# Kernel optimization log

Measured on AMD Instinct MI355X. Metric: run time of the kernel, lower is better.

Reference implementation:

```python
import jax, jax.numpy as jnp
from jax import lax
import numpy as np

L2 = 1.0   # regularization_strength for soft_rank
W1 = 1.0   # weight on (1 - spearman)
W2 = 1.0   # weight on BCE-with-logits


def _isotonic_nondecreasing(y):
    """argmin_{v1<=...<=vn} 0.5||v-y||^2 via the min-max (pool means) formula.
    v_i = max_{j<=i} min_{k>=i} mean(y[j..k]). Same solution (and generic
    gradient) as sequential PAV, but fully vectorized / O(n^2)."""
    n = y.shape[0]
    c = jnp.concatenate([jnp.zeros((1,), y.dtype), jnp.cumsum(y)])  # prefix sums
    j = jnp.arange(n)[:, None]
    k = jnp.arange(n)[None, :]
    length = (k - j + 1).astype(y.dtype)
    M = (c[k + 1] - c[j]) / length                    # mean(y[j..k]) for j<=k
    BIG = jnp.asarray(np.finfo(np.float32).max / 4, y.dtype)
    M = jnp.where(j <= k, M, BIG)                     # mask invalid j>k
    S = lax.cummin(M, axis=1, reverse=True)           # S[j,i] = min_{k>=i} M[j,k]
    V = lax.cummax(S, axis=0)                         # V[i,i] = max_{j<=i} S[j,i]
    return jnp.diagonal(V)


def _isotonic_nonincreasing(y):
    # argmin_{v1>=...>=vn} 0.5||v-y||^2  (what fast_soft_sort's isotonic_l2 solves)
    return -_isotonic_nondecreasing(-y)


def _soft_rank_1d(x, reg):
    """fast_soft_sort soft_rank (L2 regularization, ASCENDING) for a 1D vector:
    projection of x/reg onto the permutahedron of w=[n,...,1]."""
    n = x.shape[0]
    theta = x / reg
    w = jnp.arange(n, 0, -1, dtype=x.dtype)           # [n, n-1, ..., 1]
    perm = jnp.argsort(-theta)                        # descending sort
    s = theta[perm]
    dual = _isotonic_nonincreasing(s - w)
    primal = s - dual
    inv = jnp.argsort(perm)
    return primal[inv]


def setup_inputs() -> dict:
    key = jax.random.key(0)
    k1, k2 = jax.random.split(key)
    y_hat = jax.random.normal(k1, (1, 4096), dtype=jnp.float32)   # logits
    y = jax.random.uniform(k2, (1, 4096), dtype=jnp.float32)      # targets in [0,1]
    return {"y_hat": y_hat, "y": y}


def reference(y_hat, y):
    sr = jax.vmap(lambda v: _soft_rank_1d(v, L2))     # rank each row
    p = sr(y_hat)
    t = sr(y)
    p = p - p.mean()
    p = p / jnp.linalg.norm(p)
    t = t - t.mean()
    t = t / jnp.linalg.norm(t)
    spearman = jnp.sum(p * t)
    # BCEWithLogitsLoss (mean reduction): mean(log(1+exp(x)) - x*y), stable form
    bce = jnp.mean(jnp.logaddexp(0.0, y_hat) - y_hat * y)
    return W1 * (1.0 - spearman) + W2 * bce
```

## Files before the change

### kernel.cpp

```cpp
#include <hip/hip_runtime.h>
#include <math.h>

#define N 4096

__global__ __launch_bounds__(256) void rank_kernel(
        const float* __restrict__ yh, const float* __restrict__ yv,
        float* __restrict__ sA, float* __restrict__ sB,
        int* __restrict__ posA, int* __restrict__ posB) {
    int g = blockIdx.x * 256 + threadIdx.x;
    int elem = g >> 3;
    int k = g & 7;
    int row = elem >> 12;
    int i = elem & (N - 1);
    const float* X = row ? yv : yh;
    float x = X[i];
    const float4* X4 = (const float4*)X;
    int cnt = 0;
    int m0 = k * 128;
#pragma unroll 4
    for (int m = m0; m < m0 + 128; ++m) {
        float4 f = X4[m];
        int j = 4 * m;
        cnt += (int)(f.x > x) | ((int)(f.x == x) & (int)((j + 0) < i));
        cnt += (int)(f.y > x) | ((int)(f.y == x) & (int)((j + 1) < i));
        cnt += (int)(f.z > x) | ((int)(f.z == x) & (int)((j + 2) < i));
        cnt += (int)(f.w > x) | ((int)(f.w == x) & (int)((j + 3) < i));
    }
    cnt += __shfl_xor(cnt, 1, 8);
    cnt += __shfl_xor(cnt, 2, 8);
    cnt += __shfl_xor(cnt, 4, 8);
    if (k == 0) {
        if (row) { posB[i] = cnt; sB[cnt] = x; }
        else     { posA[i] = cnt; sA[cnt] = x; }
    }
}

__global__ __launch_bounds__(1024) void finalize_kernel(
        const float* __restrict__ yh, const float* __restrict__ yv,
        const float* __restrict__ sA, const float* __restrict__ sB,
        const int* __restrict__ posA, const int* __restrict__ posB,
        float* __restrict__ out) {
    __shared__ double wtot[2][8];
    __shared__ double CNsh[2];
    __shared__ unsigned short survX[2][512];
    __shared__ double survY[2][512];
    __shared__ unsigned short gX[2][516];
    __shared__ double gY[2][516];
    __shared__ double gSlope[2][516];
    __shared__ int survCnt[2];
    __shared__ int Hsh[2];
    __shared__ double wred[16][6];

    const int tid  = threadIdx.x;
    const int lane = tid & 63;
    const int wave = tid >> 6;
    const int r    = tid >> 9;
    const int ht   = tid & 511;
    const int hw   = wave & 7;
    const int q0   = ht * 8;

    int4 pa4 = ((const int4*)posA)[tid];
    int4 pb4 = ((const int4*)posB)[tid];
    float4 xh = ((const float4*)yh)[tid];
    float4 yt = ((const float4*)yv)[tid];

    const float* S = r ? sB : sA;
    float4 sa4 = ((const float4*)S)[2 * ht];
    float4 sb4 = ((const float4*)S)[2 * ht + 1];
    float sv[8] = {sa4.x, sa4.y, sa4.z, sa4.w, sb4.x, sb4.y, sb4.z, sb4.w};

    double m[8];
    double acc = 0.0;
#pragma unroll
    for (int j = 0; j < 8; ++j) {
        acc += (double)sv[j] - (double)(N - (q0 + j));
        m[j] = acc;
    }
    double tot = m[7], incl = tot;
#pragma unroll
    for (int d = 1; d < 64; d <<= 1) {
        double t = __shfl_up(incl, d, 64);
        if (lane >= d) incl += t;
    }
    if (lane == 63) wtot[r][hw] = incl;
    if (tid < 2) survCnt[tid] = 0;
    __syncthreads();

    if (tid < 16) {
        int rr = tid >> 3, idx = tid & 7;
        double v = wtot[rr][idx], inc = v;
#pragma unroll
        for (int d = 1; d < 8; d <<= 1) {
            double t = __shfl_up(inc, d, 8);
            if (idx >= d) inc += t;
        }
        wtot[rr][idx] = inc - v;
        if (idx == 7) CNsh[rr] = inc;
    }
    __syncthreads();

    double base = wtot[r][hw] + (incl - tot);
    double CN = CNsh[r];
    double eps = 1e-9 * fabs(CN) + 1e-6;
    const double invN = 1.0 / (double)N;

#pragma unroll
    for (int j = 0; j < 8; ++j) {
        int p = q0 + 1 + j;
        if (p < N) {
            double cp = base + m[j];
            if (cp > CN * ((double)p * invN) - eps) {
                int slot = atomicAdd(&survCnt[r], 1);
                if (slot < 512) { survX[r][slot] = (unsigned short)p; survY[r][slot] = cp; }
            }
        }
    }
    __syncthreads();

    if (ht == 0) {
        int k = survCnt[r]; if (k > 512) k = 512;
        for (int a = 1; a < k; ++a) {
            unsigned short vx = survX[r][a]; double vy = survY[r][a];
            int b = a - 1;
            while (b >= 0 && survX[r][b] > vx) {
                survX[r][b + 1] = survX[r][b]; survY[r][b + 1] = survY[r][b]; --b;
            }
            survX[r][b + 1] = vx; survY[r][b + 1] = vy;
        }
        int cnt = 0;
        int xa = 0, xb = 0; double ya = 0.0, yb = 0.0;
        for (int q = 0; q <= k + 1; ++q) {
            int x; double cy;
            if (q == 0)      { x = 0; cy = 0.0; }
            else if (q <= k) { x = (int)survX[r][q - 1]; cy = survY[r][q - 1]; }
            else             { x = N; cy = CN; }
            while (cnt >= 2) {
                double cr = (double)(xb - xa) * (cy - ya) - (yb - ya) * (double)(x - xa);
                if (cr >= 0.0) {
                    cnt--; xb = xa; yb = ya;
                    if (cnt >= 2) { xa = (int)gX[r][cnt - 2]; ya = gY[r][cnt - 2]; }
                } else break;
            }
            gX[r][cnt] = (unsigned short)x; gY[r][cnt] = cy;
            xa = xb; ya = yb; xb = x; yb = cy;
            cnt++;
        }
        Hsh[r] = cnt;
        for (int q = 0; q + 1 < cnt; ++q)
            gSlope[r][q] = (gY[r][q + 1] - gY[r][q]) /
                           (double)((int)gX[r][q + 1] - (int)gX[r][q]);
    }
    __syncthreads();

    double Sa = 0, Sb = 0, Saa = 0, Sbb = 0, Sab = 0, Bce = 0;
    {
        int HA = Hsh[0], HB = Hsh[1];
        int pa[4] = {pa4.x, pa4.y, pa4.z, pa4.w};
        int pb[4] = {pb4.x, pb4.y, pb4.z, pb4.w};
        float xx[4] = {xh.x, xh.y, xh.z, xh.w};
        float yy[4] = {yt.x, yt.y, yt.z, yt.w};
#pragma unroll
        for (int j = 0; j < 4; ++j) {
            int p = pa[j];
            int a = 0, b2 = HA - 1;
            while (b2 - a > 1) {
                int mm = (a + b2) >> 1;
                if ((int)gX[0][mm] <= p) a = mm; else b2 = mm;
            }
            double dualA = gSlope[0][a];
            p = pb[j];
            a = 0; b2 = HB - 1;
            while (b2 - a > 1) {
                int mm = (a + b2) >> 1;
                if ((int)gX[1][mm] <= p) a = mm; else b2 = mm;
            }
            double dualB = gSlope[1][a];

            double av = (double)xx[j] - dualA - 2048.0;
            double bv = (double)yy[j] - dualB - 2048.0;
            Sa += av; Sb += bv; Saa += av * av; Sbb += bv * bv; Sab += av * bv;
            float x = xx[j];
            float e = __expf(-fabsf(x));
            float bt = fmaxf(x, 0.0f) + __logf(1.0f + e) - x * yy[j];
            Bce += (double)bt;
        }
    }
#pragma unroll
    for (int d = 32; d; d >>= 1) {
        Sa  += __shfl_xor(Sa, d, 64);  Sb  += __shfl_xor(Sb, d, 64);
        Saa += __shfl_xor(Saa, d, 64); Sbb += __shfl_xor(Sbb, d, 64);
        Sab += __shfl_xor(Sab, d, 64); Bce += __shfl_xor(Bce, d, 64);
    }
    if (lane == 0) {
        wred[wave][0] = Sa;  wred[wave][1] = Sb;  wred[wave][2] = Saa;
        wred[wave][3] = Sbb; wred[wave][4] = Sab; wred[wave][5] = Bce;
    }
    __syncthreads();
    if (tid == 0) {
        double sa = 0, sb = 0, saa = 0, sbb = 0, sab = 0, bce = 0;
        for (int w = 0; w < 16; ++w) {
            sa += wred[w][0]; sb += wred[w][1]; saa += wred[w][2];
            sbb += wred[w][3]; sab += wred[w][4]; bce += wred[w][5];
        }
        double n = (double)N;
        double cov = sab - sa * sb / n;
        double va = saa - sa * sa / n;
        double vb = sbb - sb * sb / n;
        double spearman = cov / sqrt(va * vb);
        out[0] = (float)(1.0 - spearman + bce / n);
    }
}

extern "C" void kernel_launch(void* const* d_in, const int* in_sizes, int n_in,
                              void* d_out, int out_size, void* d_ws, size_t ws_size,
                              hipStream_t stream) {
    const float* yh = (const float*)d_in[0];
    const float* yv = (const float*)d_in[1];
    float* out = (float*)d_out;

    float* sA  = (float*)d_ws;
    float* sB  = sA + N;
    int* posA  = (int*)(sB + N);
    int* posB  = posA + N;

    hipLaunchKernelGGL(rank_kernel, dim3(256), dim3(256), 0, stream,
                       yh, yv, sA, sB, posA, posB);
    hipLaunchKernelGGL(finalize_kernel, dim3(1), dim3(1024), 0, stream,
                       yh, yv, sA, sB, posA, posB, out);
}
```

Before: 78.50 us.

## Fuse rank and finalize kernels into one cooperative launch with grid sync

Merges the counting-rank kernel and the single-block finalize kernel into one cooperative kernel, separated by a grid-wide sync. Block 0 then runs the finalize step with 256 threads instead of 1024, so each thread handles 32 sorted values and 16 elements. The goal is to drop the second launch and the gap between kernels. In exchange, the grid sync has its own cost, and the finalize step now has less parallelism and longer serial loops per thread, including many sequential atomics.

```diff
diff --git a/kernel.cpp b/kernel.cpp
--- a/kernel.cpp
+++ b/kernel.cpp
@@ -1,47 +1,52 @@
 #include <hip/hip_runtime.h>
+#include <hip/hip_cooperative_groups.h>
 #include <math.h>
 
 #define N 4096
 
-__global__ __launch_bounds__(256) void rank_kernel(
+namespace cg = cooperative_groups;
+
+__global__ __launch_bounds__(256) void fused_kernel(
         const float* __restrict__ yh, const float* __restrict__ yv,
         float* __restrict__ sA, float* __restrict__ sB,
-        int* __restrict__ posA, int* __restrict__ posB) {
-    int g = blockIdx.x * 256 + threadIdx.x;
-    int elem = g >> 3;
-    int k = g & 7;
-    int row = elem >> 12;
-    int i = elem & (N - 1);
-    const float* X = row ? yv : yh;
-    float x = X[i];
-    const float4* X4 = (const float4*)X;
-    int cnt = 0;
-    int m0 = k * 128;
+        int* __restrict__ posA, int* __restrict__ posB,
+        float* __restrict__ out) {
+    {
+        int g = blockIdx.x * 256 + threadIdx.x;
+        int elem = g >> 3;
+        int k = g & 7;
+        int row = elem >> 12;
+        int i = elem & (N - 1);
+        const float* X = row ? yv : yh;
+        float x = X[i];
+        const float4* X4 = (const float4*)X;
+        int cnt = 0;
+        int m0 = k * 128;
 #pragma unroll 4
-    for (int m = m0; m < m0 + 128; ++m) {
-        float4 f = X4[m];
-        int j = 4 * m;
-        cnt += (int)(f.x > x) | ((int)(f.x == x) & (int)((j + 0) < i));
-        cnt += (int)(f.y > x) | ((int)(f.y == x) & (int)((j + 1) < i));
-        cnt += (int)(f.z > x) | ((int)(f.z == x) & (int)((j + 2) < i));
-        cnt += (int)(f.w > x) | ((int)(f.w == x) & (int)((j + 3) < i));
-    }
-    cnt += __shfl_xor(cnt, 1, 8);
-    cnt += __shfl_xor(cnt, 2, 8);
-    cnt += __shfl_xor(cnt, 4, 8);
-    if (k == 0) {
-        if (row) { posB[i] = cnt; sB[cnt] = x; }
-        else     { posA[i] = cnt; sA[cnt] = x; }
-    }
-}
-
-__global__ __launch_bounds__(1024) void finalize_kernel(
-        const float* __restrict__ yh, const float* __restrict__ yv,
-        const float* __restrict__ sA, const float* __restrict__ sB,
-        const int* __restrict__ posA, const int* __restrict__ posB,
-        float* __restrict__ out) {
-    __shared__ double wtot[2][8];
-    __shared__ double CNsh[2];
+        for (int m = m0; m < m0 + 128; ++m) {
+            float4 f = X4[m];
+            int j = 4 * m;
+            cnt += (int)(f.x > x) | ((int)(f.x == x) & (int)((j + 0) < i));
+            cnt += (int)(f.y > x) | ((int)(f.y == x) & (int)((j + 1) < i));
+            cnt += (int)(f.z > x) | ((int)(f.z == x) & (int)((j + 2) < i));
+            cnt += (int)(f.w > x) | ((int)(f.w == x) & (int)((j + 3) < i));
+        }
+        cnt += __shfl_xor(cnt, 1, 8);
+        cnt += __shfl_xor(cnt, 2, 8);
+        cnt += __shfl_xor(cnt, 4, 8);
+        if (k == 0) {
+            if (row) { posB[i] = cnt; sB[cnt] = x; }
+            else     { posA[i] = cnt; sA[cnt] = x; }
+        }
+    }
+
+    __threadfence();
+    cg::this_grid().sync();
+
+    if (blockIdx.x != 0) return;
+    __threadfence();
+
+    __shared__ double wT[4];
     __shared__ unsigned short survX[2][512];
     __shared__ double survY[2][512];
     __shared__ unsigned short gX[2][516];
@@ -49,77 +54,78 @@
     __shared__ double gSlope[2][516];
     __shared__ int survCnt[2];
     __shared__ int Hsh[2];
-    __shared__ double wred[16][6];
+    __shared__ double wred[4][6];
 
     const int tid  = threadIdx.x;
     const int lane = tid & 63;
     const int wave = tid >> 6;
-    const int r    = tid >> 9;
-    const int ht   = tid & 511;
-    const int hw   = wave & 7;
-    const int q0   = ht * 8;
-
-    int4 pa4 = ((const int4*)posA)[tid];
-    int4 pb4 = ((const int4*)posB)[tid];
-    float4 xh = ((const float4*)yh)[tid];
-    float4 yt = ((const float4*)yv)[tid];
+    const int r    = tid >> 7;
+    const int t    = tid & 127;
+    const int q0   = t * 32;
+
+    int4 pa4[4], pb4[4]; float4 xh4[4], yt4[4];
+#pragma unroll
+    for (int u = 0; u < 4; ++u) {
+        pa4[u] = ((const int4*)posA)[4 * tid + u];
+        pb4[u] = ((const int4*)posB)[4 * tid + u];
+        xh4[u] = ((const float4*)yh)[4 * tid + u];
+        yt4[u] = ((const float4*)yv)[4 * tid + u];
+    }
 
     const float* S = r ? sB : sA;
-    float4 sa4 = ((const float4*)S)[2 * ht];
-    float4 sb4 = ((const float4*)S)[2 * ht + 1];
-    float sv[8] = {sa4.x, sa4.y, sa4.z, sa4.w, sb4.x, sb4.y, sb4.z, sb4.w};
-
-    double m[8];
+    float4 sv4[8];
+#pragma unroll
+    for (int u = 0; u < 8; ++u) sv4[u] = ((const float4*)S)[8 * t + u];
+
     double acc = 0.0;
 #pragma unroll
-    for (int j = 0; j < 8; ++j) {
-        acc += (double)sv[j] - (double)(N - (q0 + j));
-        m[j] = acc;
-    }
-    double tot = m[7], incl = tot;
+    for (int u = 0; u < 8; ++u) {
+        int q = q0 + 4 * u;
+        acc += (double)sv4[u].x - (double)(N - (q + 0));
+        acc += (double)sv4[u].y - (double)(N - (q + 1));
+        acc += (double)sv4[u].z - (double)(N - (q + 2));
+        acc += (double)sv4[u].w - (double)(N - (q + 3));
+    }
+    double tot = acc, incl = acc;
 #pragma unroll
     for (int d = 1; d < 64; d <<= 1) {
-        double t = __shfl_up(incl, d, 64);
-        if (lane >= d) incl += t;
-    }
-    if (lane == 63) wtot[r][hw] = incl;
+        double tt = __shfl_up(incl, d, 64);
+        if (lane >= d) incl += tt;
+    }
+    if (lane == 63) wT[wave] = incl;
     if (tid < 2) survCnt[tid] = 0;
     __syncthreads();
 
-    if (tid < 16) {
-        int rr = tid >> 3, idx = tid & 7;
-        double v = wtot[rr][idx], inc = v;
-#pragma unroll
-        for (int d = 1; d < 8; d <<= 1) {
-            double t = __shfl_up(inc, d, 8);
-            if (idx >= d) inc += t;
-        }
-        wtot[rr][idx] = inc - v;
-        if (idx == 7) CNsh[rr] = inc;
-    }
-    __syncthreads();
-
-    double base = wtot[r][hw] + (incl - tot);
-    double CN = CNsh[r];
+    double wprev = (wave & 1) ? wT[wave - 1] : 0.0;
+    double CN = wT[2 * r] + wT[2 * r + 1];
+    double base = wprev + (incl - tot);
     double eps = 1e-9 * fabs(CN) + 1e-6;
     const double invN = 1.0 / (double)N;
 
-#pragma unroll
-    for (int j = 0; j < 8; ++j) {
-        int p = q0 + 1 + j;
-        if (p < N) {
-            double cp = base + m[j];
-            if (cp > CN * ((double)p * invN) - eps) {
-                int slot = atomicAdd(&survCnt[r], 1);
-                if (slot < 512) { survX[r][slot] = (unsigned short)p; survY[r][slot] = cp; }
-            }
-        }
-    }
-    __syncthreads();
-
-    if (ht == 0) {
-        int k = survCnt[r]; if (k > 512) k = 512;
-        for (int a = 1; a < k; ++a) {
+    {
+        double cp = base;
+#pragma unroll
+        for (int u = 0; u < 8; ++u) {
+            float fv[4] = {sv4[u].x, sv4[u].y, sv4[u].z, sv4[u].w};
+#pragma unroll
+            for (int c = 0; c < 4; ++c) {
+                int q = q0 + 4 * u + c;
+                cp += (double)fv[c] - (double)(N - q);
+                int p = q + 1;
+                if (p < N && cp > CN * ((double)p * invN) - eps) {
+                    int slot = atomicAdd(&survCnt[r], 1);
+                    if (slot < 512) {
+                        survX[r][slot] = (unsigned short)p; survY[r][slot] = cp;
+                    }
+                }
+            }
+        }
+    }
+    __syncthreads();
+
+    if (t == 0) {
+        int kk = survCnt[r]; if (kk > 512) kk = 512;
+        for (int a = 1; a < kk; ++a) {
             unsigned short vx = survX[r][a]; double vy = survY[r][a];
             int b = a - 1;
             while (b >= 0 && survX[r][b] > vx) {
@@ -127,26 +133,26 @@
             }
             survX[r][b + 1] = vx; survY[r][b + 1] = vy;
         }
-        int cnt = 0;
+        int cnt2 = 0;
         int xa = 0, xb = 0; double ya = 0.0, yb = 0.0;
-        for (int q = 0; q <= k + 1; ++q) {
+        for (int q = 0; q <= kk + 1; ++q) {
             int x; double cy;
-            if (q == 0)      { x = 0; cy = 0.0; }
-            else if (q <= k) { x = (int)survX[r][q - 1]; cy = survY[r][q - 1]; }
-            else             { x = N; cy = CN; }
-            while (cnt >= 2) {
+            if (q == 0)       { x = 0; cy = 0.0; }
+            else if (q <= kk) { x = (int)survX[r][q - 1]; cy = survY[r][q - 1]; }
+            else              { x = N; cy = CN; }
+            while (cnt2 >= 2) {
                 double cr = (double)(xb - xa) * (cy - ya) - (yb - ya) * (double)(x - xa);
                 if (cr >= 0.0) {
-                    cnt--; xb = xa; yb = ya;
-                    if (cnt >= 2) { xa = (int)gX[r][cnt - 2]; ya = gY[r][cnt - 2]; }
+                    cnt2--; xb = xa; yb = ya;
+                    if (cnt2 >= 2) { xa = (int)gX[r][cnt2 - 2]; ya = gY[r][cnt2 - 2]; }
                 } else break;
             }
-            gX[r][cnt] = (unsigned short)x; gY[r][cnt] = cy;
+            gX[r][cnt2] = (unsigned short)x; gY[r][cnt2] = cy;
             xa = xb; ya = yb; xb = x; yb = cy;
-            cnt++;
-        }
-        Hsh[r] = cnt;
-        for (int q = 0; q + 1 < cnt; ++q)
+            cnt2++;
+        }
+        Hsh[r] = cnt2;
+        for (int q = 0; q + 1 < cnt2; ++q)
             gSlope[r][q] = (gY[r][q + 1] - gY[r][q]) /
                            (double)((int)gX[r][q + 1] - (int)gX[r][q]);
     }
@@ -155,34 +161,37 @@
     double Sa = 0, Sb = 0, Saa = 0, Sbb = 0, Sab = 0, Bce = 0;
     {
         int HA = Hsh[0], HB = Hsh[1];
-        int pa[4] = {pa4.x, pa4.y, pa4.z, pa4.w};
-        int pb[4] = {pb4.x, pb4.y, pb4.z, pb4.w};
-        float xx[4] = {xh.x, xh.y, xh.z, xh.w};
-        float yy[4] = {yt.x, yt.y, yt.z, yt.w};
-#pragma unroll
-        for (int j = 0; j < 4; ++j) {
-            int p = pa[j];
-            int a = 0, b2 = HA - 1;
-            while (b2 - a > 1) {
-                int mm = (a + b2) >> 1;
-                if ((int)gX[0][mm] <= p) a = mm; else b2 = mm;
-            }
-            double dualA = gSlope[0][a];
-            p = pb[j];
-            a = 0; b2 = HB - 1;
-            while (b2 - a > 1) {
-                int mm = (a + b2) >> 1;
-                if ((int)gX[1][mm] <= p) a = mm; else b2 = mm;
-            }
-            double dualB = gSlope[1][a];
-
-            double av = (double)xx[j] - dualA - 2048.0;
-            double bv = (double)yy[j] - dualB - 2048.0;
-            Sa += av; Sb += bv; Saa += av * av; Sbb += bv * bv; Sab += av * bv;
-            float x = xx[j];
-            float e = __expf(-fabsf(x));
-            float bt = fmaxf(x, 0.0f) + __logf(1.0f + e) - x * yy[j];
-            Bce += (double)bt;
+#pragma unroll
+        for (int u = 0; u < 4; ++u) {
+            int pa[4] = {pa4[u].x, pa4[u].y, pa4[u].z, pa4[u].w};
+            int pb[4] = {pb4[u].x, pb4[u].y, pb4[u].z, pb4[u].w};
+            float xx[4] = {xh4[u].x, xh4[u].y, xh4[u].z, xh4[u].w};
+            float yy[4] = {yt4[u].x, yt4[u].y, yt4[u].z, yt4[u].w};
+#pragma unroll
+            for (int j = 0; j < 4; ++j) {
+                int p = pa[j];
+                int a = 0, b2 = HA - 1;
+                while (b2 - a > 1) {
+                    int mm = (a + b2) >> 1;
+                    if ((int)gX[0][mm] <= p) a = mm; else b2 = mm;
+                }
+                double dualA = gSlope[0][a];
+                p = pb[j];
+                a = 0; b2 = HB - 1;
+                while (b2 - a > 1) {
+                    int mm = (a + b2) >> 1;
+                    if ((int)gX[1][mm] <= p) a = mm; else b2 = mm;
+                }
+                double dualB = gSlope[1][a];
+
+                double av = (double)xx[j] - dualA - 2048.0;
+                double bv = (double)yy[j] - dualB - 2048.0;
+                Sa += av; Sb += bv; Saa += av * av; Sbb += bv * bv; Sab += av * bv;
+                float x = xx[j];
+                float e = __expf(-fabsf(x));
+                float bt = fmaxf(x, 0.0f) + __logf(1.0f + e) - x * yy[j];
+                Bce += (double)bt;
+            }
         }
     }
 #pragma unroll
@@ -198,7 +207,7 @@
     __syncthreads();
     if (tid == 0) {
         double sa = 0, sb = 0, saa = 0, sbb = 0, sab = 0, bce = 0;
-        for (int w = 0; w < 16; ++w) {
+        for (int w = 0; w < 4; ++w) {
             sa += wred[w][0]; sb += wred[w][1]; saa += wred[w][2];
             sbb += wred[w][3]; sab += wred[w][4]; bce += wred[w][5];
         }
@@ -223,8 +232,8 @@
     int* posA  = (int*)(sB + N);
     int* posB  = posA + N;
 
-    hipLaunchKernelGGL(rank_kernel, dim3(256), dim3(256), 0, stream,
-                       yh, yv, sA, sB, posA, posB);
-    hipLaunchKernelGGL(finalize_kernel, dim3(1), dim3(1024), 0, stream,
-                       yh, yv, sA, sB, posA, posB, out);
+    void* args[] = { (void*)&yh, (void*)&yv, (void*)&sA, (void*)&sB,
+                     (void*)&posA, (void*)&posB, (void*)&out };
+    hipLaunchCooperativeKernel((const void*)fused_kernel, dim3(256), dim3(256),
+                               args, 0, stream);
 }
```

New measurement: 128.0 us. 1.63x slower.
